# Kernel optimization log

Hardware: AMD Instinct MI355X
Metric: run time of the kernel (lower is better)

## Reference

```python
import jax, jax.numpy as jnp
import numpy as np

D_MODEL = 1024
N_HEADS = 16
HEAD_DIM = D_MODEL // N_HEADS


def setup_inputs() -> dict:
    key = jax.random.key(0)
    kx, kq, kk, kv, ko = jax.random.split(key, 5)
    B, T = 4, 2048
    s = 1.0 / np.sqrt(D_MODEL)
    return {
        "x": jax.random.normal(kx, (B, T, D_MODEL), dtype=jnp.float32),
        "W_Q": jax.random.normal(kq, (D_MODEL, D_MODEL), dtype=jnp.float32) * s,
        "W_K": jax.random.normal(kk, (D_MODEL, D_MODEL), dtype=jnp.float32) * s,
        "W_V": jax.random.normal(kv, (D_MODEL, D_MODEL), dtype=jnp.float32) * s,
        "W_O": jax.random.normal(ko, (D_MODEL, D_MODEL), dtype=jnp.float32) * s,
    }


def reference(x, W_Q, W_K, W_V, W_O):
    B, T, C = x.shape
    H, hd = N_HEADS, HEAD_DIM
    # nn.Linear applies x @ W.T; W_* here are the [out,in] weight matrices.
    def proj(W):
        return (x @ W.T).reshape(B, T, H, hd).transpose(0, 2, 1, 3)  # [B,H,T,hd]
    q, k, v = proj(W_Q), proj(W_K), proj(W_V)
    scale = 1.0 / np.sqrt(hd).astype(np.float32)
    attn = jnp.einsum("bhqd,bhkd->bhqk", q, k) * scale  # [B,H,T,T]
    causal = jnp.tril(jnp.ones((T, T), dtype=bool))
    attn = jnp.where(causal, attn, -jnp.inf)
    attn = jax.nn.softmax(attn, axis=-1)
    out = jnp.einsum("bhqk,bhkd->bhqd", attn, v)  # [B,H,T,hd]
    out = out.transpose(0, 2, 1, 3).reshape(B, T, C)
    return out @ W_O.T
```

## Files before the change

kernel.cpp:

```cpp
#include <hip/hip_runtime.h>
#include <hip/hip_bf16.h>
#include <stdint.h>


typedef __attribute__((ext_vector_type(8))) short short8;
typedef __attribute__((ext_vector_type(4))) short short4v;
typedef __attribute__((ext_vector_type(4))) float floatx4;

#define LOG2E 1.4426950408889634f

__device__ __forceinline__ void gload_lds16(const void* g, void* l) {
  __builtin_amdgcn_global_load_lds(
      (const __attribute__((address_space(1))) void*)g,
      (__attribute__((address_space(3))) void*)l, 16, 0, 0);
}

__device__ __forceinline__ short f2bf(float f) {
  __hip_bfloat16 h = __float2bfloat16(f);
  return *reinterpret_cast<short*>(&h);
}

__global__ __launch_bounds__(256) void cvt_f32_bf16(const float* __restrict__ src,
                                                    short* __restrict__ dst, int n4,
                                                    float scale) {
  const int i = blockIdx.x * blockDim.x + threadIdx.x;
  if (i >= n4) return;
  const float4 v = reinterpret_cast<const float4*>(src)[i];
  short4v o;
  o.x = f2bf(v.x * scale); o.y = f2bf(v.y * scale);
  o.z = f2bf(v.z * scale); o.w = f2bf(v.w * scale);
  reinterpret_cast<short4v*>(dst)[i] = o;
}

__global__ __launch_bounds__(256) void cvt_weights(const float* __restrict__ wq,
                                                   const float* __restrict__ wk,
                                                   const float* __restrict__ wv,
                                                   const float* __restrict__ wo,
                                                   short* __restrict__ dst0,
                                                   float qscale) {
  const int y = blockIdx.y;
  const float* src = (y == 0) ? wq : (y == 1) ? wk : (y == 2) ? wv : wo;
  const float scale = (y == 0) ? qscale : 1.0f;
  short* dst = dst0 + (size_t)y * 1048576;
  const int i = blockIdx.x * blockDim.x + threadIdx.x;
  const float4 v = reinterpret_cast<const float4*>(src)[i];
  short4v o;
  o.x = f2bf(v.x * scale); o.y = f2bf(v.y * scale);
  o.z = f2bf(v.z * scale); o.w = f2bf(v.w * scale);
  reinterpret_cast<short4v*>(&dst[i * 4])[0] = o;
}

template <int MODE>
__device__ __forceinline__ void gemm_bt_body(const short* __restrict__ A,
                                             const short* __restrict__ B,
                                             void* __restrict__ Cout,
                                             int M, int N, int K, int m0, int n0) {
  __shared__ short lds_a[128 * 64];
  __shared__ short lds_b[128 * 64];
  const int tid = threadIdx.x;
  const int lane = tid & 63;
  const int w = tid >> 6;
  const int wm = w >> 1, wn = w & 1;
  const int lrow = lane & 15, lgrp = lane >> 4;

  floatx4 acc[4][4] = {};

  const int nkt = K >> 6;
  for (int kt = 0; kt < nkt; ++kt) {
    __syncthreads();
#pragma unroll
    for (int i = 0; i < 4; ++i) {
      const int chunk = i * 256 + tid;
      const int row = chunk >> 3;
      const int cb = (chunk & 7) ^ (row & 7);
      gload_lds16(A + (size_t)(m0 + row) * K + kt * 64 + cb * 8, &lds_a[chunk * 8]);
    }
#pragma unroll
    for (int i = 0; i < 4; ++i) {
      const int chunk = i * 256 + tid;
      const int row = chunk >> 3;
      const int cb = (chunk & 7) ^ (row & 7);
      gload_lds16(B + (size_t)(n0 + row) * K + kt * 64 + cb * 8, &lds_b[chunk * 8]);
    }
    __syncthreads();
#pragma unroll
    for (int ks = 0; ks < 2; ++ks) {
      short8 af[4], bfr[4];
#pragma unroll
      for (int mf = 0; mf < 4; ++mf) {
        const int row = wm * 64 + mf * 16 + lrow;
        const int cir = (ks * 4 + lgrp) ^ (row & 7);
        af[mf] = *reinterpret_cast<const short8*>(&lds_a[row * 64 + cir * 8]);
      }
#pragma unroll
      for (int nf = 0; nf < 4; ++nf) {
        const int row = wn * 64 + nf * 16 + lrow;
        const int cir = (ks * 4 + lgrp) ^ (row & 7);
        bfr[nf] = *reinterpret_cast<const short8*>(&lds_b[row * 64 + cir * 8]);
      }
#pragma unroll
      for (int mf = 0; mf < 4; ++mf)
#pragma unroll
        for (int nf = 0; nf < 4; ++nf)
          acc[mf][nf] =
              __builtin_amdgcn_mfma_f32_16x16x32_bf16(af[mf], bfr[nf], acc[mf][nf], 0, 0, 0);
    }
  }

#pragma unroll
  for (int mf = 0; mf < 4; ++mf) {
#pragma unroll
    for (int nf = 0; nf < 4; ++nf) {
      if (MODE == 2) {
        short4v pk;
#pragma unroll
        for (int r = 0; r < 4; ++r) pk[r] = f2bf(acc[mf][nf][r]);
        const int t0 = m0 + wm * 64 + mf * 16 + lgrp * 4;
        const int ch = n0 + wn * 64 + nf * 16 + lrow;
        const int bh = ((t0 >> 11) << 4) + (ch >> 6);
        short* Vt = reinterpret_cast<short*>(Cout);
        *reinterpret_cast<short4v*>(
            &Vt[(size_t)bh * 131072 + (size_t)(ch & 63) * 2048 + (t0 & 2047)]) = pk;
      } else {
#pragma unroll
        for (int r = 0; r < 4; ++r) {
          const int grow = m0 + wm * 64 + mf * 16 + lgrp * 4 + r;
          const int gcol = n0 + wn * 64 + nf * 16 + lrow;
          if (MODE == 1)
            reinterpret_cast<short*>(Cout)[(size_t)grow * N + gcol] = f2bf(acc[mf][nf][r]);
          else
            reinterpret_cast<float*>(Cout)[(size_t)grow * N + gcol] = acc[mf][nf][r];
        }
      }
    }
  }
}

__global__ __launch_bounds__(256) void gemm_qkv(
    const short* __restrict__ xb, const short* __restrict__ wq, const short* __restrict__ wk,
    const short* __restrict__ wv, short* __restrict__ Qb, short* __restrict__ Kb,
    short* __restrict__ Vt) {
  if (blockIdx.z == 0)
    gemm_bt_body<1>(xb, wq, Qb, 8192, 1024, 1024, blockIdx.x * 128, blockIdx.y * 128);
  else if (blockIdx.z == 1)
    gemm_bt_body<1>(xb, wk, Kb, 8192, 1024, 1024, blockIdx.x * 128, blockIdx.y * 128);
  else
    gemm_bt_body<2>(xb, wv, Vt, 8192, 1024, 1024, blockIdx.x * 128, blockIdx.y * 128);
}

__global__ __launch_bounds__(256) void gemm_out(const short* __restrict__ Ob,
                                                const short* __restrict__ wo,
                                                float* __restrict__ out) {
  gemm_bt_body<0>(Ob, wo, out, 8192, 1024, 1024, blockIdx.x * 128, blockIdx.y * 128);
}

__global__ __launch_bounds__(256, 4) void attn_fwd(const short* __restrict__ Q,
                                                   const short* __restrict__ K,
                                                   const short* __restrict__ Vt,
                                                   short* __restrict__ O) {
  __shared__ short lds_k[2][64 * 64];
  __shared__ short lds_v[2][64 * 64];
  __shared__ short lds_p[4][16 * 64];

  const int tid = threadIdx.x;
  const int lane = tid & 63;
  const int w = tid >> 6;
  const int lrow = lane & 15, lgrp = lane >> 4;
  const int flat = blockIdx.x;
  const int bh = flat & 63;
  const int p = flat >> 6;
  const int b = bh >> 4, h = bh & 15;

  const size_t base = (size_t)b * 2048 * 1024 + h * 64;
  const size_t vbase = (size_t)bh * 131072;

  const int srow = tid >> 3;
  const int scb = (tid & 7) ^ (srow & 7);
  const size_t koff = (size_t)srow * 1024 + scb * 8;
  const size_t voff = (size_t)srow * 2048 + scb * 8;
  short* const kd0 = &lds_k[0][tid * 8];
  short* const kd1 = &lds_k[1][tid * 8];
  short* const vd0 = &lds_v[0][tid * 8];
  short* const vd1 = &lds_v[1][tid * 8];

  auto stageK = [&](short* ldst, const short* gsrc) {
    gload_lds16(gsrc, ldst);
    gload_lds16(gsrc + 32 * 1024, ldst + 2048);
  };
  auto stageV = [&](short* ldst, const short* gsrc) {
    gload_lds16(gsrc, ldst);
    gload_lds16(gsrc + 32 * 2048, ldst + 2048);
  };

#pragma unroll 1
  for (int pass = 0; pass < 2; ++pass) {
    const int qc = pass == 0 ? (31 - p) : p;
    const int qw = qc * 64 + w * 16;
    const int nkb = qc + 1;

    short8 qf0, qf1;
    {
      const short* qp = Q + base + (size_t)(qw + lrow) * 1024 + lgrp * 8;
      qf0 = *reinterpret_cast<const short8*>(qp);
      qf1 = *reinterpret_cast<const short8*>(qp + 32);
    }

    floatx4 oacc[4] = {};
    float lsum = 0.f;

    const short* kg = K + base + koff;
    const short* vg = Vt + vbase + voff;

    auto body = [&](int kb, const short* __restrict__ ldsk,
                    const short* __restrict__ ldsv) {
      floatx4 s[4];
      __builtin_amdgcn_s_setprio(1);
#pragma unroll
      for (int nf = 0; nf < 4; ++nf) {
        const short8 kf0 = *reinterpret_cast<const short8*>(
            &ldsk[(nf * 16 + lrow) * 64 + ((lgrp) ^ (lrow & 7)) * 8]);
        const short8 kf1 = *reinterpret_cast<const short8*>(
            &ldsk[(nf * 16 + lrow) * 64 + ((4 + lgrp) ^ (lrow & 7)) * 8]);
        floatx4 z = {};
        z = __builtin_amdgcn_mfma_f32_16x16x32_bf16(kf0, qf0, z, 0, 0, 0);
        z = __builtin_amdgcn_mfma_f32_16x16x32_bf16(kf1, qf1, z, 0, 0, 0);
        s[nf] = z;
      }
      __builtin_amdgcn_s_setprio(0);

      if (kb == qc) {
#pragma unroll
        for (int nf = 0; nf < 4; ++nf)
#pragma unroll
          for (int r = 0; r < 4; ++r)
            if (nf * 16 + lgrp * 4 + r > w * 16 + lrow) s[nf][r] = -1e30f;
      }

#pragma unroll
      for (int nf = 0; nf < 4; ++nf) {
        const float p0 = __builtin_amdgcn_exp2f(s[nf][0]);
        const float p1 = __builtin_amdgcn_exp2f(s[nf][1]);
        const float p2 = __builtin_amdgcn_exp2f(s[nf][2]);
        const float p3 = __builtin_amdgcn_exp2f(s[nf][3]);
        lsum += (p0 + p1) + (p2 + p3);
        short4v pk;
        pk.x = f2bf(p0); pk.y = f2bf(p1); pk.z = f2bf(p2); pk.w = f2bf(p3);
        const int c8 = (nf * 4 + lgrp) ^ ((lrow & 7) << 1);
        *reinterpret_cast<short4v*>(&lds_p[w][lrow * 64 + c8 * 4]) = pk;
      }

      short8 pa0, pa1;
      {
        const int c0 = (lgrp) ^ (lrow & 7);
        const int c1 = (4 + lgrp) ^ (lrow & 7);
        pa0 = *reinterpret_cast<const short8*>(&lds_p[w][lrow * 64 + c0 * 8]);
        pa1 = *reinterpret_cast<const short8*>(&lds_p[w][lrow * 64 + c1 * 8]);
      }
      __builtin_amdgcn_s_setprio(1);
#pragma unroll
      for (int nf = 0; nf < 4; ++nf) {
        const short8 vf0 = *reinterpret_cast<const short8*>(
            &ldsv[(nf * 16 + lrow) * 64 + ((lgrp) ^ (lrow & 7)) * 8]);
        const short8 vf1 = *reinterpret_cast<const short8*>(
            &ldsv[(nf * 16 + lrow) * 64 + ((4 + lgrp) ^ (lrow & 7)) * 8]);
        oacc[nf] = __builtin_amdgcn_mfma_f32_16x16x32_bf16(pa0, vf0, oacc[nf], 0, 0, 0);
        oacc[nf] = __builtin_amdgcn_mfma_f32_16x16x32_bf16(pa1, vf1, oacc[nf], 0, 0, 0);
      }
      __builtin_amdgcn_s_setprio(0);
    };

    stageK(kd0, kg); kg += 65536;
    stageV(vd0, vg); vg += 64;
    __syncthreads();

#pragma unroll 1
    for (int kb = 0; kb < nkb; kb += 2) {
      if (kb + 1 < nkb) { stageK(kd1, kg); kg += 65536; stageV(vd1, vg); vg += 64; }
      body(kb, lds_k[0], lds_v[0]);
      __syncthreads();
      if (kb + 1 >= nkb) break;
      if (kb + 2 < nkb) { stageK(kd0, kg); kg += 65536; stageV(vd0, vg); vg += 64; }
      body(kb + 1, lds_k[1], lds_v[1]);
      __syncthreads();
    }

    lsum += __shfl_xor(lsum, 16, 64);
    lsum += __shfl_xor(lsum, 32, 64);
#pragma unroll
    for (int r = 0; r < 4; ++r) {
      const float linv = 1.0f / __shfl(lsum, lgrp * 4 + r, 64);
      const int t = qw + lgrp * 4 + r;
#pragma unroll
      for (int nf = 0; nf < 4; ++nf)
        O[base + (size_t)t * 1024 + nf * 16 + lrow] = f2bf(oacc[nf][r] * linv);
    }
  }
}

extern "C" void kernel_launch(void* const* d_in, const int* in_sizes, int n_in,
                              void* d_out, int out_size, void* d_ws, size_t ws_size,
                              hipStream_t stream) {
  const float* x  = (const float*)d_in[0];
  const float* Wq = (const float*)d_in[1];
  const float* Wk = (const float*)d_in[2];
  const float* Wv = (const float*)d_in[3];
  const float* Wo = (const float*)d_in[4];

  uint8_t* ws = (uint8_t*)d_ws;
  short* xb  = (short*)(ws + 0);
  short* wqb = (short*)(ws + 16777216);
  short* wkb = (short*)(ws + 18874368);
  short* wvb = (short*)(ws + 20971520);
  short* wob = (short*)(ws + 23068672);
  short* Qb  = (short*)(ws + 25165824);
  short* Kb  = (short*)(ws + 41943040);
  short* Vt  = (short*)(ws + 58720256);
  short* Ob  = (short*)(ws + 75497472);
  if (ws_size < 92274688ull) return;

  const float qscale = 0.125f * LOG2E;

  cvt_f32_bf16<<<8192, 256, 0, stream>>>(x, xb, 2097152, 1.0f);
  cvt_weights<<<dim3(1024, 4), 256, 0, stream>>>(Wq, Wk, Wv, Wo, wqb, qscale);

  gemm_qkv<<<dim3(64, 8, 3), 256, 0, stream>>>(xb, wqb, wkb, wvb, Qb, Kb, Vt);
  attn_fwd<<<1024, 256, 0, stream>>>(Qb, Kb, Vt, Ob);
  gemm_out<<<dim3(64, 8), 256, 0, stream>>>(Ob, wob, (float*)d_out);
}
```

Before: 161.6 us.

## Rewrite projection GEMMs as 256x128 double-buffered pipelined tiles with XCD-aware grid mapping

```diff
diff --git a/kernel.cpp b/kernel.cpp
--- a/kernel.cpp
+++ b/kernel.cpp
@@ -51,12 +51,14 @@
 }
 
 template <int MODE>
-__device__ __forceinline__ void gemm_bt_body(const short* __restrict__ A,
+__device__ __forceinline__ void gemm256_body(const short* __restrict__ A,
                                              const short* __restrict__ B,
                                              void* __restrict__ Cout,
-                                             int M, int N, int K, int m0, int n0) {
-  __shared__ short lds_a[128 * 64];
-  __shared__ short lds_b[128 * 64];
+                                             int m0, int n0,
+                                             short* __restrict__ la0,
+                                             short* __restrict__ la1,
+                                             short* __restrict__ lb0,
+                                             short* __restrict__ lb1) {
   const int tid = threadIdx.x;
   const int lane = tid & 63;
   const int w = tid >> 6;
@@ -65,46 +67,89 @@
 
   floatx4 acc[4][4] = {};
 
-  const int nkt = K >> 6;
-  for (int kt = 0; kt < nkt; ++kt) {
-    __syncthreads();
-#pragma unroll
-    for (int i = 0; i < 4; ++i) {
-      const int chunk = i * 256 + tid;
-      const int row = chunk >> 3;
-      const int cb = (chunk & 7) ^ (row & 7);
-      gload_lds16(A + (size_t)(m0 + row) * K + kt * 64 + cb * 8, &lds_a[chunk * 8]);
-    }
-#pragma unroll
-    for (int i = 0; i < 4; ++i) {
-      const int chunk = i * 256 + tid;
-      const int row = chunk >> 3;
-      const int cb = (chunk & 7) ^ (row & 7);
-      gload_lds16(B + (size_t)(n0 + row) * K + kt * 64 + cb * 8, &lds_b[chunk * 8]);
-    }
-    __syncthreads();
-#pragma unroll
-    for (int ks = 0; ks < 2; ++ks) {
-      short8 af[4], bfr[4];
-#pragma unroll
-      for (int mf = 0; mf < 4; ++mf) {
-        const int row = wm * 64 + mf * 16 + lrow;
-        const int cir = (ks * 4 + lgrp) ^ (row & 7);
-        af[mf] = *reinterpret_cast<const short8*>(&lds_a[row * 64 + cir * 8]);
-      }
-#pragma unroll
-      for (int nf = 0; nf < 4; ++nf) {
-        const int row = wn * 64 + nf * 16 + lrow;
-        const int cir = (ks * 4 + lgrp) ^ (row & 7);
-        bfr[nf] = *reinterpret_cast<const short8*>(&lds_b[row * 64 + cir * 8]);
-      }
+  const int srow = tid >> 3;
+  const int scb = (tid & 7) ^ (srow & 7);
+  const short* ag = A + (size_t)(m0 + srow) * 1024 + scb * 8;
+  const short* bg = B + (size_t)(n0 + srow) * 1024 + scb * 8;
+
+  auto stage_a3 = [&](short* la) {
+    gload_lds16(ag, la + tid * 8);
+    gload_lds16(ag + 64 * 1024, la + (512 + tid) * 8);
+    gload_lds16(ag + 128 * 1024, la + (1024 + tid) * 8);
+  };
+  auto stage_b3 = [&](short* la, short* lb) {
+    gload_lds16(ag + 192 * 1024, la + (1536 + tid) * 8);
+    gload_lds16(bg, lb + tid * 8);
+    gload_lds16(bg + 64 * 1024, lb + (512 + tid) * 8);
+  };
+
+  short8 af[2][4];
+  auto loadA = [&](const short* la) {
+#pragma unroll
+    for (int mf = 0; mf < 4; ++mf) {
+      const int row = wm * 64 + mf * 16 + lrow;
+#pragma unroll
+      for (int kk = 0; kk < 2; ++kk)
+        af[kk][mf] = *reinterpret_cast<const short8*>(
+            &la[row * 64 + (((kk * 4 + lgrp) ^ (row & 7)) * 8)]);
+    }
+  };
+  auto half = [&](const short* lb, int nh) {
+    short8 bf[2][2];
+#pragma unroll
+    for (int nf = 0; nf < 2; ++nf) {
+      const int row = wn * 64 + (nh * 2 + nf) * 16 + lrow;
+#pragma unroll
+      for (int kk = 0; kk < 2; ++kk)
+        bf[kk][nf] = *reinterpret_cast<const short8*>(
+            &lb[row * 64 + (((kk * 4 + lgrp) ^ (row & 7)) * 8)]);
+    }
+    __builtin_amdgcn_s_setprio(1);
+#pragma unroll
+    for (int kk = 0; kk < 2; ++kk)
 #pragma unroll
       for (int mf = 0; mf < 4; ++mf)
 #pragma unroll
-        for (int nf = 0; nf < 4; ++nf)
-          acc[mf][nf] =
-              __builtin_amdgcn_mfma_f32_16x16x32_bf16(af[mf], bfr[nf], acc[mf][nf], 0, 0, 0);
-    }
+        for (int nf = 0; nf < 2; ++nf)
+          acc[mf][nh * 2 + nf] = __builtin_amdgcn_mfma_f32_16x16x32_bf16(
+              af[kk][mf], bf[kk][nf], acc[mf][nh * 2 + nf], 0, 0, 0);
+    __builtin_amdgcn_s_setprio(0);
+  };
+
+  auto iter_pre = [&](const short* lac, const short* lbc, short* lan, short* lbn) {
+    stage_a3(lan);
+    asm volatile("s_waitcnt vmcnt(3)" ::: "memory");
+    __builtin_amdgcn_s_barrier();
+    __builtin_amdgcn_sched_barrier(0);
+    loadA(lac);
+    half(lbc, 0);
+    stage_b3(lan, lbn);
+    ag += 64; bg += 64;
+    half(lbc, 1);
+    __builtin_amdgcn_sched_barrier(0);
+    __builtin_amdgcn_s_barrier();
+    __builtin_amdgcn_sched_barrier(0);
+  };
+
+  stage_a3(la0);
+  stage_b3(la0, lb0);
+  ag += 64; bg += 64;
+
+#pragma unroll 1
+  for (int kt = 0; kt < 12; kt += 2) {
+    iter_pre(la0, lb0, la1, lb1);
+    iter_pre(la1, lb1, la0, lb0);
+  }
+  iter_pre(la0, lb0, la1, lb1);
+  iter_pre(la1, lb1, la0, lb0);
+  iter_pre(la0, lb0, la1, lb1);
+  {
+    asm volatile("s_waitcnt vmcnt(0)" ::: "memory");
+    __builtin_amdgcn_s_barrier();
+    __builtin_amdgcn_sched_barrier(0);
+    loadA(la1);
+    half(lb1, 0);
+    half(lb1, 1);
   }
 
 #pragma unroll
@@ -127,31 +172,46 @@
           const int grow = m0 + wm * 64 + mf * 16 + lgrp * 4 + r;
           const int gcol = n0 + wn * 64 + nf * 16 + lrow;
           if (MODE == 1)
-            reinterpret_cast<short*>(Cout)[(size_t)grow * N + gcol] = f2bf(acc[mf][nf][r]);
+            reinterpret_cast<short*>(Cout)[(size_t)grow * 1024 + gcol] = f2bf(acc[mf][nf][r]);
           else
-            reinterpret_cast<float*>(Cout)[(size_t)grow * N + gcol] = acc[mf][nf][r];
+            reinterpret_cast<float*>(Cout)[(size_t)grow * 1024 + gcol] = acc[mf][nf][r];
         }
       }
     }
   }
 }
 
-__global__ __launch_bounds__(256) void gemm_qkv(
+__global__ __launch_bounds__(512) void gemm_qkv(
     const short* __restrict__ xb, const short* __restrict__ wq, const short* __restrict__ wk,
     const short* __restrict__ wv, short* __restrict__ Qb, short* __restrict__ Kb,
     short* __restrict__ Vt) {
-  if (blockIdx.z == 0)
-    gemm_bt_body<1>(xb, wq, Qb, 8192, 1024, 1024, blockIdx.x * 128, blockIdx.y * 128);
-  else if (blockIdx.z == 1)
-    gemm_bt_body<1>(xb, wk, Kb, 8192, 1024, 1024, blockIdx.x * 128, blockIdx.y * 128);
+  __shared__ short lds_a[2][256 * 64];
+  __shared__ short lds_b[2][128 * 64];
+  const int flat = blockIdx.x;
+  const int xcd = flat & 7, rest = flat >> 3;
+  const int nblk = rest & 7, pg = rest >> 3;
+  const int panel = pg * 8 + xcd;
+  const int m = panel & 31, z = panel >> 5;
+  const int m0 = m * 256, n0 = nblk * 128;
+  if (z == 0)
+    gemm256_body<1>(xb, wq, Qb, m0, n0, lds_a[0], lds_a[1], lds_b[0], lds_b[1]);
+  else if (z == 1)
+    gemm256_body<1>(xb, wk, Kb, m0, n0, lds_a[0], lds_a[1], lds_b[0], lds_b[1]);
   else
-    gemm_bt_body<2>(xb, wv, Vt, 8192, 1024, 1024, blockIdx.x * 128, blockIdx.y * 128);
-}
-
-__global__ __launch_bounds__(256) void gemm_out(const short* __restrict__ Ob,
+    gemm256_body<2>(xb, wv, Vt, m0, n0, lds_a[0], lds_a[1], lds_b[0], lds_b[1]);
+}
+
+__global__ __launch_bounds__(512) void gemm_out(const short* __restrict__ Ob,
                                                 const short* __restrict__ wo,
                                                 float* __restrict__ out) {
-  gemm_bt_body<0>(Ob, wo, out, 8192, 1024, 1024, blockIdx.x * 128, blockIdx.y * 128);
+  __shared__ short lds_a[2][256 * 64];
+  __shared__ short lds_b[2][128 * 64];
+  const int flat = blockIdx.x;
+  const int xcd = flat & 7, rest = flat >> 3;
+  const int nblk = rest & 7, pg = rest >> 3;
+  const int panel = pg * 8 + xcd;
+  gemm256_body<0>(Ob, wo, out, panel * 256, nblk * 128,
+                  lds_a[0], lds_a[1], lds_b[0], lds_b[1]);
 }
 
 __global__ __launch_bounds__(256, 4) void attn_fwd(const short* __restrict__ Q,
@@ -323,7 +383,7 @@
   cvt_f32_bf16<<<8192, 256, 0, stream>>>(x, xb, 2097152, 1.0f);
   cvt_weights<<<dim3(1024, 4), 256, 0, stream>>>(Wq, Wk, Wv, Wo, wqb, qscale);
 
-  gemm_qkv<<<dim3(64, 8, 3), 256, 0, stream>>>(xb, wqb, wkb, wvb, Qb, Kb, Vt);
+  gemm_qkv<<<768, 512, 0, stream>>>(xb, wqb, wkb, wvb, Qb, Kb, Vt);
   attn_fwd<<<1024, 256, 0, stream>>>(Qb, Kb, Vt, Ob);
-  gemm_out<<<dim3(64, 8), 256, 0, stream>>>(Ob, wob, (float*)d_out);
-}
+  gemm_out<<<256, 512, 0, stream>>>(Ob, wob, (float*)d_out);
+}
```

After: 156.3 us. 3.3% less time.
